# Performance work log

Hardware: AMD Instinct MI355X
Metric: run time of the kernel (lower is better)

The kernel has to match this reference:

```python
import jax, jax.numpy as jnp
import numpy as np

D_MODEL = 1024
NUM_HEADS = 16
HEAD_DIM = D_MODEL // NUM_HEADS


def setup_inputs() -> dict:
    key = jax.random.key(0)
    k_x, k_wqkv, k_bqkv, k_wfc, k_bfc = jax.random.split(key, 5)
    scale_in = 1.0 / np.sqrt(D_MODEL)
    return {
        "x": jax.random.normal(k_x, (2, 2048, D_MODEL), dtype=jnp.float32),
        # torch nn.Linear stores weight as [out_features, in_features]
        "w_qkv": jax.random.uniform(k_wqkv, (3 * D_MODEL, D_MODEL), jnp.float32, -scale_in, scale_in),
        "b_qkv": jax.random.uniform(k_bqkv, (3 * D_MODEL,), jnp.float32, -scale_in, scale_in),
        "w_fc": jax.random.uniform(k_wfc, (D_MODEL, D_MODEL), jnp.float32, -scale_in, scale_in),
        "b_fc": jax.random.uniform(k_bfc, (D_MODEL,), jnp.float32, -scale_in, scale_in),
    }


def reference(x, w_qkv, b_qkv, w_fc, b_fc):
    B, S, _ = x.shape
    # fused QKV projection: [B,S,3*d_model]
    qkv = jnp.einsum("bsd,ed->bse", x, w_qkv) + b_qkv
    # [B,S,H,3*head_dim] -> [B,H,S,3*head_dim]
    qkv = qkv.reshape(B, S, NUM_HEADS, 3 * HEAD_DIM).transpose(0, 2, 1, 3)
    Q, K, V = jnp.split(qkv, 3, axis=-1)  # each [B,H,S,head_dim]
    scores = jnp.einsum("bhqd,bhkd->bhqk", Q, K) / np.sqrt(HEAD_DIM).astype(np.float32)
    attention = jax.nn.softmax(scores, axis=-1)  # [B,H,S,S]
    values = jnp.einsum("bhqk,bhkd->bhqd", attention, V)
    # [B,H,S,head_dim] -> [B,S,d_model]
    values = values.transpose(0, 2, 1, 3).reshape(B, S, D_MODEL)
    out = jnp.einsum("bsd,ed->bse", values, w_fc) + b_fc
    return out
```

## Files before the change

### kernel.cpp

```cpp
#include <hip/hip_runtime.h>
#include <hip/hip_bf16.h>

#define D_MODEL 1024
#define NH 16
#define HD 64
#define BATCH 2
#define SEQ 2048

typedef __attribute__((ext_vector_type(8))) short short8;
typedef __attribute__((ext_vector_type(4))) float floatx4;

static __device__ __forceinline__ short f2bf(float f) {
    __hip_bfloat16 h = __float2bfloat16(f);
    return *reinterpret_cast<short*>(&h);
}
static __device__ __forceinline__ unsigned int pk2bf(float a, float b) {
    float2 t; t.x = a; t.y = b;
    __hip_bfloat162 h2 = __float22bfloat162_rn(t);
    return *reinterpret_cast<unsigned int*>(&h2);
}

__global__ __launch_bounds__(256) void cvt_all(
    const float* __restrict__ x, const float* __restrict__ wq,
    const float* __restrict__ wf,
    short* __restrict__ Xb, short* __restrict__ Wqb, short* __restrict__ Wfb)
{
    int i = blockIdx.x * 256 + threadIdx.x;
    const float* src; short* dst; int off;
    if (i < 524288)      { src = x;  dst = Xb;  off = i; }
    else if (i < 917504) { src = wq; dst = Wqb; off = i - 524288; }
    else                 { src = wf; dst = Wfb; off = i - 917504; }
    float4 a = *reinterpret_cast<const float4*>(src + off * 8);
    float4 b = *reinterpret_cast<const float4*>(src + off * 8 + 4);
    short8 o;
    o[0] = f2bf(a.x); o[1] = f2bf(a.y); o[2] = f2bf(a.z); o[3] = f2bf(a.w);
    o[4] = f2bf(b.x); o[5] = f2bf(b.y); o[6] = f2bf(b.z); o[7] = f2bf(b.w);
    *reinterpret_cast<short8*>(dst + off * 8) = o;
}

__global__ __launch_bounds__(256) void qkv_gemm(
    const short* __restrict__ X, const short* __restrict__ W,
    const float* __restrict__ bias,
    short* __restrict__ Qs, short* __restrict__ Ks, short* __restrict__ Vt_g)
{
    __shared__ __align__(16) short As[128][72];
    __shared__ __align__(16) short Bs[128][72];
    const int tid = threadIdx.x;
    const int m0 = blockIdx.y * 128;
    const int n0 = blockIdx.x * 128;
    const int bi = m0 >> 11, sl0 = m0 & 2047;
    const int w = tid >> 6, lane = tid & 63;
    const int quad = lane >> 4, l15 = lane & 15;
    const int wm2 = w >> 1, wn2 = w & 1;

    floatx4 acc[4][4];
#pragma unroll
    for (int i = 0; i < 4; i++)
#pragma unroll
        for (int j = 0; j < 4; j++) acc[i][j] = (floatx4)0.0f;

    for (int k0 = 0; k0 < 1024; k0 += 64) {
        __syncthreads();
#pragma unroll
        for (int i = 0; i < 4; i++) {
            int c = tid + i * 256;
            int row = c >> 3, ck = c & 7;
            *reinterpret_cast<uint4*>(&As[row][ck * 8]) =
                *reinterpret_cast<const uint4*>(&X[(m0 + row) * 1024 + k0 + ck * 8]);
            *reinterpret_cast<uint4*>(&Bs[row][ck * 8]) =
                *reinterpret_cast<const uint4*>(&W[(n0 + row) * 1024 + k0 + ck * 8]);
        }
        __syncthreads();
#pragma unroll
        for (int kk = 0; kk < 2; kk++) {
            short8 a[4], b[4];
#pragma unroll
            for (int t = 0; t < 4; t++) {
                a[t] = *reinterpret_cast<const short8*>(&As[wm2 * 64 + t * 16 + l15][kk * 32 + quad * 8]);
                b[t] = *reinterpret_cast<const short8*>(&Bs[wn2 * 64 + t * 16 + l15][kk * 32 + quad * 8]);
            }
#pragma unroll
            for (int mt = 0; mt < 4; mt++)
#pragma unroll
                for (int nt = 0; nt < 4; nt++)
                    acc[mt][nt] = __builtin_amdgcn_mfma_f32_16x16x32_bf16(
                        a[mt], b[nt], acc[mt][nt], 0, 0, 0);
        }
    }

    __syncthreads();
    short* T = &As[0][0];
#pragma unroll
    for (int half = 0; half < 2; half++) {
        const int colg0 = n0 + half * 64;
        const int h = colg0 / 192;
        const int t = (colg0 % 192) / 64;
        if (wn2 == half) {
#pragma unroll
            for (int nt = 0; nt < 4; nt++) {
                int jj = nt * 16 + l15;
                float bv = bias[colg0 + jj];
#pragma unroll
                for (int mt = 0; mt < 4; mt++) {
#pragma unroll
                    for (int r = 0; r < 4; r++) {
                        int ml = wm2 * 64 + mt * 16 + quad * 4 + r;
                        float v = acc[mt][nt][r] + bv;
                        if (t == 0) v *= 0.18033688f;
                        if (t < 2) As[ml][jj] = f2bf(v);
                        else       T[jj * 136 + ml] = f2bf(v);
                    }
                }
            }
        }
        __syncthreads();
        if (t < 2) {
            short* dst = (t == 0) ? Qs : Ks;
#pragma unroll
            for (int i = 0; i < 4; i++) {
                int c = tid + i * 256;
                int row = c >> 3, ck = c & 7;
                uint4 u = *reinterpret_cast<const uint4*>(&As[row][ck * 8]);
                *reinterpret_cast<uint4*>(
                    &dst[((size_t)(bi * NH + h) * SEQ + sl0 + row) * HD + ck * 8]) = u;
            }
        } else {
#pragma unroll
            for (int i = 0; i < 4; i++) {
                int c = tid + i * 256;
                int d = c >> 4, ck = c & 15;
                uint4 u = *reinterpret_cast<const uint4*>(&T[d * 136 + ck * 8]);
                *reinterpret_cast<uint4*>(
                    &Vt_g[((size_t)(bi * NH + h) * HD + d) * SEQ + sl0 + ck * 8]) = u;
            }
        }
        __syncthreads();
    }
}

__global__ __launch_bounds__(256) void attn_kernel(
    const short* __restrict__ Qs, const short* __restrict__ Ks,
    const short* __restrict__ Vt_g, short* __restrict__ attn)
{
    __shared__ __align__(16) short Kl[2][64][72];
    __shared__ __align__(16) short Vt[2][64][72];
    __shared__ __align__(16) short Pl[4][32][72];
    __shared__ float Ls[128];

    const int tid = threadIdx.x;
    const int w = tid >> 6, lane = tid & 63;
    const int quad = lane >> 4, l15 = lane & 15;
    const int q0 = blockIdx.x * 128;
    const int h = blockIdx.y, bi = blockIdx.z;
    const int bh = bi * NH + h;
    const int kbase = bh * SEQ * HD;
    const int vbase = bh * HD * SEQ;

    const int kr0 = tid >> 3,         kc0 = (tid & 7) * 8;
    const int kr1 = (tid + 256) >> 3, kc1 = (tid & 7) * 8;

    short8 aq[2][2];
#pragma unroll
    for (int qt2 = 0; qt2 < 2; qt2++) {
        const short* qp = Qs + kbase + (q0 + w * 32 + qt2 * 16 + l15) * HD;
#pragma unroll
        for (int c = 0; c < 2; c++)
            aq[qt2][c] = *reinterpret_cast<const short8*>(qp + c * 32 + quad * 8);
    }

    {
        uint4 ka = *reinterpret_cast<const uint4*>(&Ks[kbase + kr0 * HD + kc0]);
        uint4 kb = *reinterpret_cast<const uint4*>(&Ks[kbase + kr1 * HD + kc1]);
        uint4 va = *reinterpret_cast<const uint4*>(&Vt_g[vbase + kr0 * SEQ + kc0]);
        uint4 vb = *reinterpret_cast<const uint4*>(&Vt_g[vbase + kr1 * SEQ + kc1]);
        *reinterpret_cast<uint4*>(&Kl[0][kr0][kc0]) = ka;
        *reinterpret_cast<uint4*>(&Kl[0][kr1][kc1]) = kb;
        *reinterpret_cast<uint4*>(&Vt[0][kr0][kc0]) = va;
        *reinterpret_cast<uint4*>(&Vt[0][kr1][kc1]) = vb;
    }

    float l_acc[2] = {0.f, 0.f};
    floatx4 o[2][4];
#pragma unroll
    for (int mt = 0; mt < 2; mt++)
#pragma unroll
        for (int nt = 0; nt < 4; nt++) o[mt][nt] = (floatx4)0.0f;

    for (int it = 0; it < SEQ / 64; it++) {
        const int cur = it & 1;
        __syncthreads();

        uint4 kna, knb, vna, vnb;
        const bool more = (it + 1 < SEQ / 64);
        if (more) {
            int ktn = (it + 1) * 64;
            kna = *reinterpret_cast<const uint4*>(&Ks[kbase + (ktn + kr0) * HD + kc0]);
            knb = *reinterpret_cast<const uint4*>(&Ks[kbase + (ktn + kr1) * HD + kc1]);
            vna = *reinterpret_cast<const uint4*>(&Vt_g[vbase + kr0 * SEQ + ktn + kc0]);
            vnb = *reinterpret_cast<const uint4*>(&Vt_g[vbase + kr1 * SEQ + ktn + kc1]);
        }

        floatx4 sf[4][2];
#pragma unroll
        for (int kt2 = 0; kt2 < 4; kt2++)
#pragma unroll
            for (int qt2 = 0; qt2 < 2; qt2++) sf[kt2][qt2] = (floatx4)0.0f;
#pragma unroll
        for (int c = 0; c < 2; c++) {
#pragma unroll
            for (int kt2 = 0; kt2 < 4; kt2++) {
                short8 bk = *reinterpret_cast<const short8*>(
                    &Kl[cur][kt2 * 16 + l15][c * 32 + quad * 8]);
#pragma unroll
                for (int qt2 = 0; qt2 < 2; qt2++)
                    sf[kt2][qt2] = __builtin_amdgcn_mfma_f32_16x16x32_bf16(
                        bk, aq[qt2][c], sf[kt2][qt2], 0, 0, 0);
            }
        }

#pragma unroll
        for (int kt2 = 0; kt2 < 4; kt2++) {
#pragma unroll
            for (int qt2 = 0; qt2 < 2; qt2++) {
                float e0 = exp2f(sf[kt2][qt2][0]);
                float e1 = exp2f(sf[kt2][qt2][1]);
                float e2 = exp2f(sf[kt2][qt2][2]);
                float e3 = exp2f(sf[kt2][qt2][3]);
                l_acc[qt2] += (e0 + e1) + (e2 + e3);
                uint2 p;
                p.x = pk2bf(e0, e1);
                p.y = pk2bf(e2, e3);
                *reinterpret_cast<uint2*>(&Pl[w][qt2 * 16 + l15][kt2 * 16 + quad * 4]) = p;
            }
        }
        asm volatile("s_waitcnt lgkmcnt(0)" ::: "memory");

#pragma unroll
        for (int c = 0; c < 2; c++) {
#pragma unroll
            for (int mt = 0; mt < 2; mt++) {
                short8 ap = *reinterpret_cast<const short8*>(
                    &Pl[w][mt * 16 + l15][c * 32 + quad * 8]);
#pragma unroll
                for (int nt = 0; nt < 4; nt++) {
                    short8 bv = *reinterpret_cast<const short8*>(
                        &Vt[cur][nt * 16 + l15][c * 32 + quad * 8]);
                    o[mt][nt] = __builtin_amdgcn_mfma_f32_16x16x32_bf16(
                        ap, bv, o[mt][nt], 0, 0, 0);
                }
            }
        }

        if (more) {
            int nxt = 1 - cur;
            *reinterpret_cast<uint4*>(&Kl[nxt][kr0][kc0]) = kna;
            *reinterpret_cast<uint4*>(&Kl[nxt][kr1][kc1]) = knb;
            *reinterpret_cast<uint4*>(&Vt[nxt][kr0][kc0]) = vna;
            *reinterpret_cast<uint4*>(&Vt[nxt][kr1][kc1]) = vnb;
        }
    }

#pragma unroll
    for (int qt2 = 0; qt2 < 2; qt2++) {
        l_acc[qt2] += __shfl_xor(l_acc[qt2], 16);
        l_acc[qt2] += __shfl_xor(l_acc[qt2], 32);
    }
    if (quad == 0) {
        Ls[w * 32 + l15] = l_acc[0];
        Ls[w * 32 + 16 + l15] = l_acc[1];
    }
    asm volatile("s_waitcnt lgkmcnt(0)" ::: "memory");

#pragma unroll
    for (int mt = 0; mt < 2; mt++) {
#pragma unroll
        for (int r = 0; r < 4; r++) {
            int ql = w * 32 + mt * 16 + quad * 4 + r;
            float lt = Ls[ql];
#pragma unroll
            for (int nt = 0; nt < 4; nt++) {
                attn[(bi * SEQ + q0 + ql) * D_MODEL + h * HD + nt * 16 + l15] =
                    f2bf(o[mt][nt][r] / lt);
            }
        }
    }
}

__global__ __launch_bounds__(256) void fc_gemm(
    const short* __restrict__ A, const short* __restrict__ W,
    const float* __restrict__ bias, float* __restrict__ out)
{
    __shared__ __align__(16) short As[128][72];
    __shared__ __align__(16) short Bs[64][72];
    const int tid = threadIdx.x;
    const int m0 = blockIdx.y * 128;
    const int n0 = blockIdx.x * 64;
    const int w = tid >> 6, lane = tid & 63;
    const int quad = lane >> 4, l15 = lane & 15;
    const int wm2 = w >> 1, wn2 = w & 1;

    floatx4 acc[4][2];
#pragma unroll
    for (int i = 0; i < 4; i++)
#pragma unroll
        for (int j = 0; j < 2; j++) acc[i][j] = (floatx4)0.0f;

    for (int k0 = 0; k0 < 1024; k0 += 64) {
        __syncthreads();
#pragma unroll
        for (int i = 0; i < 4; i++) {
            int c = tid + i * 256;
            int row = c >> 3, ck = c & 7;
            *reinterpret_cast<uint4*>(&As[row][ck * 8]) =
                *reinterpret_cast<const uint4*>(&A[(m0 + row) * 1024 + k0 + ck * 8]);
        }
#pragma unroll
        for (int i = 0; i < 2; i++) {
            int c = tid + i * 256;
            int row = c >> 3, ck = c & 7;
            *reinterpret_cast<uint4*>(&Bs[row][ck * 8]) =
                *reinterpret_cast<const uint4*>(&W[(n0 + row) * 1024 + k0 + ck * 8]);
        }
        __syncthreads();
#pragma unroll
        for (int kk = 0; kk < 2; kk++) {
            short8 a[4], b[2];
#pragma unroll
            for (int i = 0; i < 4; i++)
                a[i] = *reinterpret_cast<const short8*>(&As[wm2 * 64 + i * 16 + l15][kk * 32 + quad * 8]);
#pragma unroll
            for (int j = 0; j < 2; j++)
                b[j] = *reinterpret_cast<const short8*>(&Bs[wn2 * 32 + j * 16 + l15][kk * 32 + quad * 8]);
#pragma unroll
            for (int mt = 0; mt < 4; mt++)
#pragma unroll
                for (int nt = 0; nt < 2; nt++)
                    acc[mt][nt] = __builtin_amdgcn_mfma_f32_16x16x32_bf16(
                        a[mt], b[nt], acc[mt][nt], 0, 0, 0);
        }
    }

#pragma unroll
    for (int nt = 0; nt < 2; nt++) {
        int col = n0 + wn2 * 32 + nt * 16 + l15;
        float bv = bias[col];
#pragma unroll
        for (int mt = 0; mt < 4; mt++) {
#pragma unroll
            for (int r = 0; r < 4; r++) {
                int row = m0 + wm2 * 64 + mt * 16 + quad * 4 + r;
                out[row * 1024 + col] = acc[mt][nt][r] + bv;
            }
        }
    }
}

extern "C" void kernel_launch(void* const* d_in, const int* in_sizes, int n_in,
                              void* d_out, int out_size, void* d_ws, size_t ws_size,
                              hipStream_t stream) {
    const float* x     = (const float*)d_in[0];
    const float* w_qkv = (const float*)d_in[1];
    const float* b_qkv = (const float*)d_in[2];
    const float* w_fc  = (const float*)d_in[3];
    const float* b_fc  = (const float*)d_in[4];
    float* out = (float*)d_out;

    const size_t M4 = 4u * 1024 * 1024;
    short* Xb    = (short*)d_ws;
    short* Wqb   = Xb + M4;
    short* Wfb   = Wqb + 3u * 1024 * 1024;
    short* Qs    = Wfb + 1024 * 1024;
    short* Ks    = Qs + M4;
    short* Vt_g  = Ks + M4;
    short* attnb = Xb;

    cvt_all<<<4096, 256, 0, stream>>>(x, w_qkv, w_fc, Xb, Wqb, Wfb);
    qkv_gemm<<<dim3(24, 32), 256, 0, stream>>>(Xb, Wqb, b_qkv, Qs, Ks, Vt_g);
    attn_kernel<<<dim3(16, 16, 2), 256, 0, stream>>>(Qs, Ks, Vt_g, attnb);
    fc_gemm<<<dim3(16, 32), 256, 0, stream>>>(attnb, Wfb, b_fc, out);
}
```

Baseline: 228.9 us.

## Split attention over key halves and merge partial results in a combine kernel

The attention kernel now splits the key sequence into two halves, doubling the grid to 1024 blocks so more CUs stay busy. Each half writes unnormalized fp16 partial outputs and row sums, and a new combine kernel adds them, normalizes, and writes bf16. Row sums are now computed with an extra MFMA against a ones vector instead of scalar adds, and the double-buffered K/V prefetch is replaced by single-buffered loads with two barriers per tile. The cost is an extra kernel launch, extra memory traffic for the partials, and fp16 range risk on the unnormalized accumulators.

```diff
diff --git a/kernel.cpp b/kernel.cpp
--- a/kernel.cpp
+++ b/kernel.cpp
@@ -1,5 +1,6 @@
 #include <hip/hip_runtime.h>
 #include <hip/hip_bf16.h>
+#include <hip/hip_fp16.h>
 
 #define D_MODEL 1024
 #define NH 16
@@ -9,6 +10,7 @@
 
 typedef __attribute__((ext_vector_type(8))) short short8;
 typedef __attribute__((ext_vector_type(4))) float floatx4;
+typedef __attribute__((ext_vector_type(8))) _Float16 half8;
 
 static __device__ __forceinline__ short f2bf(float f) {
     __hip_bfloat16 h = __float2bfloat16(f);
@@ -138,27 +140,33 @@
     }
 }
 
-__global__ __launch_bounds__(256) void attn_kernel(
+__global__ __launch_bounds__(256, 4) void attn_kernel(
     const short* __restrict__ Qs, const short* __restrict__ Ks,
-    const short* __restrict__ Vt_g, short* __restrict__ attn)
-{
-    __shared__ __align__(16) short Kl[2][64][72];
-    __shared__ __align__(16) short Vt[2][64][72];
+    const short* __restrict__ Vt_g,
+    _Float16* __restrict__ Opart, float* __restrict__ lpart)
+{
+    __shared__ __align__(16) short Kl[64][72];
+    __shared__ __align__(16) short Vt[64][72];
     __shared__ __align__(16) short Pl[4][32][72];
-    __shared__ float Ls[128];
 
     const int tid = threadIdx.x;
     const int w = tid >> 6, lane = tid & 63;
     const int quad = lane >> 4, l15 = lane & 15;
-    const int q0 = blockIdx.x * 128;
+    const int bx = blockIdx.x;
+    const int khalf = bx & 1;
+    const int q0 = (bx >> 1) * 128;
     const int h = blockIdx.y, bi = blockIdx.z;
     const int bh = bi * NH + h;
     const int kbase = bh * SEQ * HD;
     const int vbase = bh * HD * SEQ;
+    const int kt0 = khalf * (SEQ / 2);
 
     const int kr0 = tid >> 3,         kc0 = (tid & 7) * 8;
     const int kr1 = (tid + 256) >> 3, kc1 = (tid & 7) * 8;
 
+    const short8 onesv = {(short)0x3F80, (short)0x3F80, (short)0x3F80, (short)0x3F80,
+                          (short)0x3F80, (short)0x3F80, (short)0x3F80, (short)0x3F80};
+
     short8 aq[2][2];
 #pragma unroll
     for (int qt2 = 0; qt2 < 2; qt2++) {
@@ -168,37 +176,26 @@
             aq[qt2][c] = *reinterpret_cast<const short8*>(qp + c * 32 + quad * 8);
     }
 
-    {
-        uint4 ka = *reinterpret_cast<const uint4*>(&Ks[kbase + kr0 * HD + kc0]);
-        uint4 kb = *reinterpret_cast<const uint4*>(&Ks[kbase + kr1 * HD + kc1]);
-        uint4 va = *reinterpret_cast<const uint4*>(&Vt_g[vbase + kr0 * SEQ + kc0]);
-        uint4 vb = *reinterpret_cast<const uint4*>(&Vt_g[vbase + kr1 * SEQ + kc1]);
-        *reinterpret_cast<uint4*>(&Kl[0][kr0][kc0]) = ka;
-        *reinterpret_cast<uint4*>(&Kl[0][kr1][kc1]) = kb;
-        *reinterpret_cast<uint4*>(&Vt[0][kr0][kc0]) = va;
-        *reinterpret_cast<uint4*>(&Vt[0][kr1][kc1]) = vb;
-    }
-
-    float l_acc[2] = {0.f, 0.f};
-    floatx4 o[2][4];
-#pragma unroll
-    for (int mt = 0; mt < 2; mt++)
+    floatx4 o[2][4], ol[2];
+#pragma unroll
+    for (int mt = 0; mt < 2; mt++) {
+        ol[mt] = (floatx4)0.0f;
 #pragma unroll
         for (int nt = 0; nt < 4; nt++) o[mt][nt] = (floatx4)0.0f;
-
-    for (int it = 0; it < SEQ / 64; it++) {
-        const int cur = it & 1;
-        __syncthreads();
-
-        uint4 kna, knb, vna, vnb;
-        const bool more = (it + 1 < SEQ / 64);
-        if (more) {
-            int ktn = (it + 1) * 64;
-            kna = *reinterpret_cast<const uint4*>(&Ks[kbase + (ktn + kr0) * HD + kc0]);
-            knb = *reinterpret_cast<const uint4*>(&Ks[kbase + (ktn + kr1) * HD + kc1]);
-            vna = *reinterpret_cast<const uint4*>(&Vt_g[vbase + kr0 * SEQ + ktn + kc0]);
-            vnb = *reinterpret_cast<const uint4*>(&Vt_g[vbase + kr1 * SEQ + ktn + kc1]);
-        }
+    }
+
+    for (int it = 0; it < SEQ / 128; it++) {
+        const int kt = kt0 + it * 64;
+        __syncthreads();
+        *reinterpret_cast<uint4*>(&Kl[kr0][kc0]) =
+            *reinterpret_cast<const uint4*>(&Ks[kbase + (kt + kr0) * HD + kc0]);
+        *reinterpret_cast<uint4*>(&Kl[kr1][kc1]) =
+            *reinterpret_cast<const uint4*>(&Ks[kbase + (kt + kr1) * HD + kc1]);
+        *reinterpret_cast<uint4*>(&Vt[kr0][kc0]) =
+            *reinterpret_cast<const uint4*>(&Vt_g[vbase + kr0 * SEQ + kt + kc0]);
+        *reinterpret_cast<uint4*>(&Vt[kr1][kc1]) =
+            *reinterpret_cast<const uint4*>(&Vt_g[vbase + kr1 * SEQ + kt + kc1]);
+        __syncthreads();
 
         floatx4 sf[4][2];
 #pragma unroll
@@ -210,7 +207,7 @@
 #pragma unroll
             for (int kt2 = 0; kt2 < 4; kt2++) {
                 short8 bk = *reinterpret_cast<const short8*>(
-                    &Kl[cur][kt2 * 16 + l15][c * 32 + quad * 8]);
+                    &Kl[kt2 * 16 + l15][c * 32 + quad * 8]);
 #pragma unroll
                 for (int qt2 = 0; qt2 < 2; qt2++)
                     sf[kt2][qt2] = __builtin_amdgcn_mfma_f32_16x16x32_bf16(
@@ -222,14 +219,9 @@
         for (int kt2 = 0; kt2 < 4; kt2++) {
 #pragma unroll
             for (int qt2 = 0; qt2 < 2; qt2++) {
-                float e0 = exp2f(sf[kt2][qt2][0]);
-                float e1 = exp2f(sf[kt2][qt2][1]);
-                float e2 = exp2f(sf[kt2][qt2][2]);
-                float e3 = exp2f(sf[kt2][qt2][3]);
-                l_acc[qt2] += (e0 + e1) + (e2 + e3);
                 uint2 p;
-                p.x = pk2bf(e0, e1);
-                p.y = pk2bf(e2, e3);
+                p.x = pk2bf(exp2f(sf[kt2][qt2][0]), exp2f(sf[kt2][qt2][1]));
+                p.y = pk2bf(exp2f(sf[kt2][qt2][2]), exp2f(sf[kt2][qt2][3]));
                 *reinterpret_cast<uint2*>(&Pl[w][qt2 * 16 + l15][kt2 * 16 + quad * 4]) = p;
             }
         }
@@ -237,53 +229,60 @@
 
 #pragma unroll
         for (int c = 0; c < 2; c++) {
+            short8 vf[4];
+#pragma unroll
+            for (int nt = 0; nt < 4; nt++)
+                vf[nt] = *reinterpret_cast<const short8*>(
+                    &Vt[nt * 16 + l15][c * 32 + quad * 8]);
 #pragma unroll
             for (int mt = 0; mt < 2; mt++) {
                 short8 ap = *reinterpret_cast<const short8*>(
                     &Pl[w][mt * 16 + l15][c * 32 + quad * 8]);
 #pragma unroll
-                for (int nt = 0; nt < 4; nt++) {
-                    short8 bv = *reinterpret_cast<const short8*>(
-                        &Vt[cur][nt * 16 + l15][c * 32 + quad * 8]);
+                for (int nt = 0; nt < 4; nt++)
                     o[mt][nt] = __builtin_amdgcn_mfma_f32_16x16x32_bf16(
-                        ap, bv, o[mt][nt], 0, 0, 0);
-                }
-            }
-        }
-
-        if (more) {
-            int nxt = 1 - cur;
-            *reinterpret_cast<uint4*>(&Kl[nxt][kr0][kc0]) = kna;
-            *reinterpret_cast<uint4*>(&Kl[nxt][kr1][kc1]) = knb;
-            *reinterpret_cast<uint4*>(&Vt[nxt][kr0][kc0]) = vna;
-            *reinterpret_cast<uint4*>(&Vt[nxt][kr1][kc1]) = vnb;
-        }
-    }
-
-#pragma unroll
-    for (int qt2 = 0; qt2 < 2; qt2++) {
-        l_acc[qt2] += __shfl_xor(l_acc[qt2], 16);
-        l_acc[qt2] += __shfl_xor(l_acc[qt2], 32);
-    }
-    if (quad == 0) {
-        Ls[w * 32 + l15] = l_acc[0];
-        Ls[w * 32 + 16 + l15] = l_acc[1];
-    }
-    asm volatile("s_waitcnt lgkmcnt(0)" ::: "memory");
+                        ap, vf[nt], o[mt][nt], 0, 0, 0);
+                ol[mt] = __builtin_amdgcn_mfma_f32_16x16x32_bf16(
+                    ap, onesv, ol[mt], 0, 0, 0);
+            }
+        }
+    }
 
 #pragma unroll
     for (int mt = 0; mt < 2; mt++) {
 #pragma unroll
         for (int r = 0; r < 4; r++) {
-            int ql = w * 32 + mt * 16 + quad * 4 + r;
-            float lt = Ls[ql];
-#pragma unroll
-            for (int nt = 0; nt < 4; nt++) {
-                attn[(bi * SEQ + q0 + ql) * D_MODEL + h * HD + nt * 16 + l15] =
-                    f2bf(o[mt][nt][r] / lt);
-            }
-        }
-    }
+            int ql = q0 + w * 32 + mt * 16 + quad * 4 + r;
+            size_t base = (size_t)khalf * (4096u * 1024u) +
+                          ((size_t)bi * SEQ + ql) * D_MODEL + h * HD;
+#pragma unroll
+            for (int nt = 0; nt < 4; nt++)
+                Opart[base + nt * 16 + l15] = (_Float16)o[mt][nt][r];
+            if (l15 == 0)
+                lpart[khalf * 65536 + bh * SEQ + ql] = ol[mt][r];
+        }
+    }
+}
+
+__global__ __launch_bounds__(256) void combine_kernel(
+    const _Float16* __restrict__ O, const float* __restrict__ lp,
+    short* __restrict__ attnb)
+{
+    int i = blockIdx.x * 256 + threadIdx.x;
+    int m = i >> 7;
+    int e0 = (i & 127) * 8;
+    int bi = m >> 11, s = m & 2047, h = e0 >> 6;
+    int bh = bi * NH + h;
+    float l = lp[bh * SEQ + s] + lp[65536 + bh * SEQ + s];
+    float rl = 1.0f / l;
+    size_t off = (size_t)m * D_MODEL + e0;
+    half8 a = *reinterpret_cast<const half8*>(O + off);
+    half8 b = *reinterpret_cast<const half8*>(O + 4096u * 1024u + off);
+    short8 out;
+#pragma unroll
+    for (int j = 0; j < 8; j++)
+        out[j] = f2bf(((float)a[j] + (float)b[j]) * rl);
+    *reinterpret_cast<short8*>(attnb + off) = out;
 }
 
 __global__ __launch_bounds__(256) void fc_gemm(
@@ -365,17 +364,21 @@
     const float* b_fc  = (const float*)d_in[4];
     float* out = (float*)d_out;
 
-    const size_t M4 = 4u * 1024 * 1024;
-    short* Xb    = (short*)d_ws;
-    short* Wqb   = Xb + M4;
-    short* Wfb   = Wqb + 3u * 1024 * 1024;
-    short* Qs    = Wfb + 1024 * 1024;
-    short* Ks    = Qs + M4;
-    short* Vt_g  = Ks + M4;
-    short* attnb = Xb;
+    const size_t M1 = 1024u * 1024u;
+    short* ws = (short*)d_ws;
+    short* Qs    = ws;
+    short* Ks    = ws + 4 * M1;
+    short* Vt_g  = ws + 8 * M1;
+    short* Wfb   = ws + 12 * M1;
+    short* Xb    = ws + 13 * M1;
+    short* Wqb   = ws + 17 * M1;
+    _Float16* Opart = (_Float16*)(ws + 13 * M1);
+    float* lpart = (float*)(ws + 21 * M1);
+    short* attnb = Qs;
 
     cvt_all<<<4096, 256, 0, stream>>>(x, w_qkv, w_fc, Xb, Wqb, Wfb);
     qkv_gemm<<<dim3(24, 32), 256, 0, stream>>>(Xb, Wqb, b_qkv, Qs, Ks, Vt_g);
-    attn_kernel<<<dim3(16, 16, 2), 256, 0, stream>>>(Qs, Ks, Vt_g, attnb);
+    attn_kernel<<<dim3(32, 16, 2), 256, 0, stream>>>(Qs, Ks, Vt_g, Opart, lpart);
+    combine_kernel<<<2048, 256, 0, stream>>>(Opart, lpart, attnb);
     fc_gemm<<<dim3(16, 32), 256, 0, stream>>>(attnb, Wfb, b_fc, out);
 }
```

Result: faster. 222.3 us (-2.9%).
